# Performance work log

Measured on AMD Instinct MI355X. Metric: run time of the kernel, lower is better.

Reference implementation:

```python
import jax, jax.numpy as jnp
import numpy as np

PATCH = 14   # vision_config.patch_size
MERGE = 2    # spatial_merge_size
D = 1024     # vision_config.hidden_size
# pixel (H, W) per image; all dims divisible by PATCH*MERGE = 28
IMAGE_SIZES = np.array([[1540, 1232], [1120, 1540], [896, 1260],
                        [1540, 1540], [1260, 896], [728, 1540]], dtype=np.int64)


def setup_inputs() -> dict:
    key = jax.random.key(0)
    k1, k2 = jax.random.split(key)
    hs = IMAGE_SIZES[:, 0] // PATCH
    ws = IMAGE_SIZES[:, 1] // PATCH
    total_tokens = int(np.sum(hs * ws))  # 47820
    image_features = jax.random.normal(k1, (total_tokens, D), dtype=jnp.float32)
    # nn.Linear(D*MERGE**2 -> D, bias=False): weight [D, D*MERGE**2]
    weight = jax.random.normal(k2, (D, D * MERGE * MERGE), dtype=jnp.float32) * 0.02
    return {"image_features": image_features, "weight": weight,
            "image_sizes": IMAGE_SIZES}


def _merge_patches(image_features, image_sizes):
    """Per-image unfold(kernel=stride=MERGE) -> [n_blocks, D*MERGE^2], concatenated."""
    m = MERGE
    d = image_features.shape[-1]
    sizes = np.asarray(image_sizes)
    hs = sizes[:, 0] // PATCH
    ws = sizes[:, 1] // PATCH
    offsets = np.concatenate([[0], np.cumsum(hs * ws)])
    grids = []
    for i in range(sizes.shape[0]):
        h, w = int(hs[i]), int(ws[i])
        x = jax.lax.dynamic_slice_in_dim(image_features, int(offsets[i]), h * w, 0)
        # [h, w, d] -> blocks of m x m; torch unfold layout is (d, kh, kw) channel-major
        x = x.reshape(h // m, m, w // m, m, d)
        x = x.transpose(0, 2, 4, 1, 3)           # [h/m, w/m, d, m, m]
        x = x.reshape((h // m) * (w // m), d * m * m)
        grids.append(x)
    return jnp.concatenate(grids, axis=0)        # [sum(h*w)/m^2, d*m^2]


def reference(image_features, weight, image_sizes):
    merged = _merge_patches(image_features, image_sizes)
    return merged @ weight.T                     # [N_merged, D]
```

## Files before the change

### kernel.cpp

```cpp
#include <hip/hip_runtime.h>
#include <hip/hip_bf16.h>
#include <stdint.h>

#define K_DIM 4096
#define N_DIM 1024
#define M_TOT 11955

#define BM 128
#define BN 128
#define BK 64

__constant__ int c_wm[6]     = {44, 55, 45, 55, 32, 55};
__constant__ int c_w[6]      = {88, 110, 90, 110, 64, 110};
__constant__ int c_tokoff[6] = {0, 9680, 18480, 24240, 36340, 42100};
__constant__ int c_blkoff[6] = {0, 2420, 4620, 6060, 9085, 10525};

typedef __attribute__((ext_vector_type(8))) short bf16x8;
typedef __attribute__((ext_vector_type(4))) float f32x4;

__global__ __launch_bounds__(256) void cvt_feat(
    const float* __restrict__ src, __hip_bfloat16* __restrict__ dst)
{
    const size_t idx = (size_t)blockIdx.x * 256 + threadIdx.x;
    const float4* s = (const float4*)src + idx * 2;
    float4 a = s[0], b = s[1];
    union { __hip_bfloat16 h[8]; uint4 u; } pk;
    pk.h[0] = __float2bfloat16(a.x); pk.h[1] = __float2bfloat16(a.y);
    pk.h[2] = __float2bfloat16(a.z); pk.h[3] = __float2bfloat16(a.w);
    pk.h[4] = __float2bfloat16(b.x); pk.h[5] = __float2bfloat16(b.y);
    pk.h[6] = __float2bfloat16(b.z); pk.h[7] = __float2bfloat16(b.w);
    *((uint4*)dst + idx) = pk.u;
}

__global__ __launch_bounds__(256) void wperm_cvt(
    const float* __restrict__ src, __hip_bfloat16* __restrict__ dst)
{
    const int n = blockIdx.x >> 1;
    const int t = (blockIdx.x & 1) * 256 + threadIdx.x;
    const float* row = src + (size_t)n * K_DIM + t * 8;
    float4 a = *(const float4*)row;
    float4 b = *(const float4*)(row + 4);
    const float va[8] = {a.x, a.y, a.z, a.w, b.x, b.y, b.z, b.w};
    __hip_bfloat16* drow = dst + (size_t)n * K_DIM + 2 * t;
#pragma unroll
    for (int seg = 0; seg < 4; ++seg) {
        __hip_bfloat162 h = __float22bfloat162_rn(
            make_float2(va[seg], va[4 + seg]));
        *(__hip_bfloat162*)(drow + seg * 1024) = h;
    }
}

__global__ __launch_bounds__(256) void gemm_bt(
    const __hip_bfloat16* __restrict__ A,
    const __hip_bfloat16* __restrict__ Wp,
    float* __restrict__ C)
{
    __shared__ __align__(16) __hip_bfloat16 lA[BM * BK];
    __shared__ __align__(16) __hip_bfloat16 lB[BN * BK];

    const int tid  = threadIdx.x;
    const int lane = tid & 63;
    const int wave = tid >> 6;
    const int m0 = blockIdx.y * BM;
    const int n0 = blockIdx.x * BN;
    const int wm = (wave >> 1) * 64;
    const int wn = (wave & 1) * 64;
    const int al = lane & 15;
    const int q  = lane >> 4;
    const int al7 = al & 7;

    int t00[4], ww[4];
    const __hip_bfloat16* pBbase[4];
#pragma unroll
    for (int j = 0; j < 4; ++j) {
        const int c = tid + j * 256;
        const int row = c >> 3;
        const int g = (c & 7) ^ (row & 7);
        int gm = m0 + row; if (gm > M_TOT - 1) gm = M_TOT - 1;
        int img = 0;
#pragma unroll
        for (int u = 1; u < 6; ++u) if (gm >= c_blkoff[u]) img = u;
        const int bi = gm - c_blkoff[img];
        const int wmrg = c_wm[img];
        const int gi = bi / wmrg;
        const int gj = bi - gi * wmrg;
        ww[j]  = c_w[img];
        t00[j] = c_tokoff[img] + 2 * gi * ww[j] + 2 * gj;
        t00[j] = t00[j];
        pBbase[j] = Wp + (size_t)(n0 + row) * K_DIM + g * 8;
        ww[j] |= (g << 16);
    }

    f32x4 acc[4][4];
#pragma unroll
    for (int i = 0; i < 4; ++i)
#pragma unroll
        for (int j = 0; j < 4; ++j)
            acc[i][j] = (f32x4){0.f, 0.f, 0.f, 0.f};

#pragma unroll
    for (int seg = 0; seg < 4; ++seg) {
        const int kh = seg >> 1, kw = seg & 1;
        const __hip_bfloat16* pA[4];
        const __hip_bfloat16* pB[4];
#pragma unroll
        for (int j = 0; j < 4; ++j) {
            const int w = ww[j] & 0xffff;
            const int g = ww[j] >> 16;
            pA[j] = A + (size_t)(t00[j] + kh * w + kw) * N_DIM + g * 8;
            pB[j] = pBbase[j] + seg * 1024;
        }
        for (int k2 = 0; k2 < 1024; k2 += BK) {
#pragma unroll
            for (int j = 0; j < 4; ++j)
                __builtin_amdgcn_global_load_lds(
                    (const __attribute__((address_space(1))) void*)(pA[j] + k2),
                    (__attribute__((address_space(3))) void*)(lA + (tid + j * 256) * 8),
                    16, 0, 0);
#pragma unroll
            for (int j = 0; j < 4; ++j)
                __builtin_amdgcn_global_load_lds(
                    (const __attribute__((address_space(1))) void*)(pB[j] + k2),
                    (__attribute__((address_space(3))) void*)(lB + (tid + j * 256) * 8),
                    16, 0, 0);
            __syncthreads();

            bf16x8 af[4], bfr[4];
#pragma unroll
            for (int ks = 0; ks < 2; ++ks) {
#pragma unroll
                for (int mi = 0; mi < 4; ++mi) {
                    const int r = wm + mi * 16 + al;
                    const int p = (ks * 4 + q) ^ al7;
                    af[mi] = *(const bf16x8*)(lA + r * BK + p * 8);
                }
#pragma unroll
                for (int ni = 0; ni < 4; ++ni) {
                    const int r = wn + ni * 16 + al;
                    const int p = (ks * 4 + q) ^ al7;
                    bfr[ni] = *(const bf16x8*)(lB + r * BK + p * 8);
                }
#pragma unroll
                for (int mi = 0; mi < 4; ++mi)
#pragma unroll
                    for (int ni = 0; ni < 4; ++ni)
                        acc[mi][ni] = __builtin_amdgcn_mfma_f32_16x16x32_bf16(
                            af[mi], bfr[ni], acc[mi][ni], 0, 0, 0);
            }
            __syncthreads();
        }
    }

#pragma unroll
    for (int mi = 0; mi < 4; ++mi) {
        const int row = m0 + wm + mi * 16 + q * 4;
#pragma unroll
        for (int ni = 0; ni < 4; ++ni) {
            const int col = n0 + wn + ni * 16 + al;
            float* cp = C + (size_t)row * N_DIM + col;
#pragma unroll
            for (int rg = 0; rg < 4; ++rg) {
                if (row + rg < M_TOT) cp[(size_t)rg * N_DIM] = acc[mi][ni][rg];
            }
        }
    }
}

extern "C" void kernel_launch(void* const* d_in, const int* in_sizes, int n_in,
                              void* d_out, int out_size, void* d_ws, size_t ws_size,
                              hipStream_t stream)
{
    const float* feat = (const float*)d_in[0];
    const float* wgt  = (const float*)d_in[1];
    float* out = (float*)d_out;

    __hip_bfloat16* featbf = (__hip_bfloat16*)d_ws;
    __hip_bfloat16* wp = (__hip_bfloat16*)((char*)d_ws +
                         (size_t)47820 * N_DIM * sizeof(__hip_bfloat16));

    cvt_feat<<<23910, 256, 0, stream>>>(feat, featbf);
    wperm_cvt<<<2048, 256, 0, stream>>>(wgt, wp);

    dim3 grid(N_DIM / BN, (M_TOT + BM - 1) / BM);
    gemm_bt<<<grid, 256, 0, stream>>>(featbf, wp, out);
}
```

Before: 438.0 us.

## Fuse feature fp32-to-bf16 conversion into GEMM A-tile loads with XCD-aware tile mapping

Removes the separate feature conversion kernel and its bf16 workspace round trip; the GEMM now loads fp32 features into registers, converts them to bf16 and stores them into LDS. Blocks are remapped to a 1D grid so that consecutive tiles sharing the same M rows land on the same XCD, improving L2 reuse of the fp32 A data. The tradeoff is twice the A-load bytes per tile and synchronous register-staged loads in place of async direct-to-LDS loads, which may expose more latency in the main loop.

```diff
diff --git a/kernel.cpp b/kernel.cpp
--- a/kernel.cpp
+++ b/kernel.cpp
@@ -9,6 +9,8 @@
 #define BM 128
 #define BN 128
 #define BK 64
+#define NWG_M 94
+#define NWG 752
 
 __constant__ int c_wm[6]     = {44, 55, 45, 55, 32, 55};
 __constant__ int c_w[6]      = {88, 110, 90, 110, 64, 110};
@@ -17,20 +19,6 @@
 
 typedef __attribute__((ext_vector_type(8))) short bf16x8;
 typedef __attribute__((ext_vector_type(4))) float f32x4;
-
-__global__ __launch_bounds__(256) void cvt_feat(
-    const float* __restrict__ src, __hip_bfloat16* __restrict__ dst)
-{
-    const size_t idx = (size_t)blockIdx.x * 256 + threadIdx.x;
-    const float4* s = (const float4*)src + idx * 2;
-    float4 a = s[0], b = s[1];
-    union { __hip_bfloat16 h[8]; uint4 u; } pk;
-    pk.h[0] = __float2bfloat16(a.x); pk.h[1] = __float2bfloat16(a.y);
-    pk.h[2] = __float2bfloat16(a.z); pk.h[3] = __float2bfloat16(a.w);
-    pk.h[4] = __float2bfloat16(b.x); pk.h[5] = __float2bfloat16(b.y);
-    pk.h[6] = __float2bfloat16(b.z); pk.h[7] = __float2bfloat16(b.w);
-    *((uint4*)dst + idx) = pk.u;
-}
 
 __global__ __launch_bounds__(256) void wperm_cvt(
     const float* __restrict__ src, __hip_bfloat16* __restrict__ dst)
@@ -50,19 +38,26 @@
     }
 }
 
-__global__ __launch_bounds__(256) void gemm_bt(
-    const __hip_bfloat16* __restrict__ A,
+__global__ __launch_bounds__(256) void gemm_fused(
+    const float* __restrict__ A,
     const __hip_bfloat16* __restrict__ Wp,
     float* __restrict__ C)
 {
     __shared__ __align__(16) __hip_bfloat16 lA[BM * BK];
     __shared__ __align__(16) __hip_bfloat16 lB[BN * BK];
 
+    const int f    = blockIdx.x;
+    const int xcd  = f & 7;
+    const int slot = f >> 3;
+    const int gidx = xcd * NWG_M + slot;
+    const int mt   = gidx >> 3;
+    const int nt   = gidx & 7;
+    const int m0 = mt * BM;
+    const int n0 = nt * BN;
+
     const int tid  = threadIdx.x;
     const int lane = tid & 63;
     const int wave = tid >> 6;
-    const int m0 = blockIdx.y * BM;
-    const int n0 = blockIdx.x * BN;
     const int wm = (wave >> 1) * 64;
     const int wn = (wave & 1) * 64;
     const int al = lane & 15;
@@ -84,11 +79,10 @@
         const int wmrg = c_wm[img];
         const int gi = bi / wmrg;
         const int gj = bi - gi * wmrg;
-        ww[j]  = c_w[img];
-        t00[j] = c_tokoff[img] + 2 * gi * ww[j] + 2 * gj;
-        t00[j] = t00[j];
+        const int w = c_w[img];
+        t00[j] = c_tokoff[img] + 2 * gi * w + 2 * gj;
         pBbase[j] = Wp + (size_t)(n0 + row) * K_DIM + g * 8;
-        ww[j] |= (g << 16);
+        ww[j] = w | (g << 16);
     }
 
     f32x4 acc[4][4];
@@ -101,7 +95,7 @@
 #pragma unroll
     for (int seg = 0; seg < 4; ++seg) {
         const int kh = seg >> 1, kw = seg & 1;
-        const __hip_bfloat16* pA[4];
+        const float* pA[4];
         const __hip_bfloat16* pB[4];
 #pragma unroll
         for (int j = 0; j < 4; ++j) {
@@ -114,15 +108,25 @@
 #pragma unroll
             for (int j = 0; j < 4; ++j)
                 __builtin_amdgcn_global_load_lds(
-                    (const __attribute__((address_space(1))) void*)(pA[j] + k2),
-                    (__attribute__((address_space(3))) void*)(lA + (tid + j * 256) * 8),
-                    16, 0, 0);
-#pragma unroll
-            for (int j = 0; j < 4; ++j)
-                __builtin_amdgcn_global_load_lds(
                     (const __attribute__((address_space(1))) void*)(pB[j] + k2),
                     (__attribute__((address_space(3))) void*)(lB + (tid + j * 256) * 8),
                     16, 0, 0);
+            float4 ra[4][2];
+#pragma unroll
+            for (int j = 0; j < 4; ++j) {
+                const float4* s = (const float4*)(pA[j] + k2);
+                ra[j][0] = s[0];
+                ra[j][1] = s[1];
+            }
+#pragma unroll
+            for (int j = 0; j < 4; ++j) {
+                union { __hip_bfloat162 h2[4]; uint4 u; } pk;
+                pk.h2[0] = __float22bfloat162_rn(make_float2(ra[j][0].x, ra[j][0].y));
+                pk.h2[1] = __float22bfloat162_rn(make_float2(ra[j][0].z, ra[j][0].w));
+                pk.h2[2] = __float22bfloat162_rn(make_float2(ra[j][1].x, ra[j][1].y));
+                pk.h2[3] = __float22bfloat162_rn(make_float2(ra[j][1].z, ra[j][1].w));
+                *(uint4*)(lA + (size_t)(tid + j * 256) * 8) = pk.u;
+            }
             __syncthreads();
 
             bf16x8 af[4], bfr[4];
@@ -174,13 +178,8 @@
     const float* wgt  = (const float*)d_in[1];
     float* out = (float*)d_out;
 
-    __hip_bfloat16* featbf = (__hip_bfloat16*)d_ws;
-    __hip_bfloat16* wp = (__hip_bfloat16*)((char*)d_ws +
-                         (size_t)47820 * N_DIM * sizeof(__hip_bfloat16));
+    __hip_bfloat16* wp = (__hip_bfloat16*)d_ws;
 
-    cvt_feat<<<23910, 256, 0, stream>>>(feat, featbf);
     wperm_cvt<<<2048, 256, 0, stream>>>(wgt, wp);
-
-    dim3 grid(N_DIM / BN, (M_TOT + BM - 1) / BM);
-    gemm_bt<<<grid, 256, 0, stream>>>(featbf, wp, out);
+    gemm_fused<<<NWG, 256, 0, stream>>>(feat, wp, out);
 }
```

Result: slower. 463.9 us (+5.9%).
